# Kernel optimization log

Hardware: AMD Instinct MI355X
Metric: run time of the kernel (lower is better)

Reference implementation:

```python
import jax, jax.numpy as jnp
import numpy as np

N, T, H, F, NZ, G = 768, 8, 128, 128, 64, 64
D = H + F + NZ  # DecoderFC input dim = 320


def _init(key, shape, scale=0.05):
    return jax.random.normal(key, shape, dtype=jnp.float32) * scale


def setup_inputs() -> dict:
    key = jax.random.key(0)
    ks = jax.random.split(key, 16)
    return dict(
        obsv_4d=jax.random.normal(ks[0], (N, T, 4), jnp.float32),
        noise=jax.random.normal(ks[1], (N, NZ), jnp.float32),
        W_emb=_init(ks[2], (H, 4)), b_emb=jnp.zeros((H,), jnp.float32),
        W_ih=_init(ks[3], (4 * H, H)), W_hh=_init(ks[4], (4 * H, H)),
        b_ih=jnp.zeros((4 * H,), jnp.float32), b_hh=jnp.zeros((4 * H,), jnp.float32),
        Wf1=_init(ks[5], (32, 3)), bf1=jnp.zeros((32,), jnp.float32),
        Wf2=_init(ks[6], (64, 32)), bf2=jnp.zeros((64,), jnp.float32),
        Wf3=_init(ks[7], (F, 64)), bf3=jnp.zeros((F,), jnp.float32),
        Wa=_init(ks[8], (F, H)), ba=jnp.zeros((F,), jnp.float32),
        Wd1=_init(ks[9], (D, D)), bd1=jnp.zeros((D,), jnp.float32),
        Wd2=_init(ks[10], (D // 2, D)), bd2=jnp.zeros((D // 2,), jnp.float32),
        Wd3=_init(ks[11], (D // 4, D // 2)), bd3=jnp.zeros((D // 4,), jnp.float32),
        Wd4=_init(ks[12], (2, D // 4)), bd4=jnp.zeros((2,), jnp.float32),
        n_next=12, group_size=G,
    )


def _lstm_cell(h, c, x, W_ih, W_hh, b_ih, b_hh):
    # PyTorch gate order: i, f, g, o
    z = x @ W_ih.T + h @ W_hh.T + b_ih + b_hh
    i, f, g, o = jnp.split(z, 4, axis=-1)
    c = jax.nn.sigmoid(f) * c + jax.nn.sigmoid(i) * jnp.tanh(g)
    h = jax.nn.sigmoid(o) * jnp.tanh(c)
    return h, c


def _social_features(x_last):
    # x_last: [N,4] = (px, py, vx, vy) at last observed step
    Dx = x_last[:, None, :] - x_last[None, :, :]          # [N,N,4]
    Dp, Dv = Dx[..., :2], Dx[..., 2:]
    l2 = jnp.linalg.norm(Dp, axis=2)                      # pairwise distance
    v = jnp.broadcast_to(x_last[:, None, 2:], Dp.shape)   # velocity of agent i
    cos = jnp.sum(Dp * v, -1) / (jnp.linalg.norm(Dp, axis=2) * jnp.linalg.norm(v, axis=2) + 1e-6)
    ttca = -jnp.sum(Dp * Dv, -1) / (jnp.sum(Dv * Dv, -1) + 1e-6)
    dca = jnp.linalg.norm(Dp + ttca[..., None] * Dv, axis=2)
    return jnp.stack([l2, cos, dca], axis=2)              # [N,N,3]


def _attention(f, h, Wa, ba, group_size):
    # Block-diagonal social attention pooling over equal-size sub-batches.
    n = h.shape[0]
    B = n // group_size
    Wh = h @ Wa.T + ba                                    # [N,F]
    fg = f.reshape(B, group_size, B, group_size, -1)
    fg = fg[jnp.arange(B), :, jnp.arange(B)]              # [B,G,G,F] diag blocks
    Whg = Wh.reshape(B, group_size, -1)
    hg = h.reshape(B, group_size, -1)
    sigma = jnp.einsum('bijf,bjf->bij', fg, Whg)          # [B,G,G]
    eye = jnp.eye(group_size, dtype=bool)
    sigma = jnp.where(eye[None], -1000.0, sigma)          # mask self, as in torch code
    attn = jax.nn.softmax(sigma, axis=2)
    S = jnp.einsum('bij,bjh->bih', attn, hg)              # [B,G,H]
    return S.reshape(n, -1)


def reference(obsv_4d, noise, W_emb, b_emb, W_ih, W_hh, b_ih, b_hh,
              Wf1, bf1, Wf2, bf2, Wf3, bf3, Wa, ba,
              Wd1, bd1, Wd2, bd2, Wd3, bd3, Wd4, bd4, n_next, group_size):
    n = obsv_4d.shape[0]
    hdim = W_hh.shape[1]
    # ---- encoder LSTM over observed trajectory ----
    x = obsv_4d @ W_emb.T + b_emb                         # [N,T,H]

    def enc_step(carry, xt):
        h, c = carry
        h, c = _lstm_cell(h, c, xt, W_ih, W_hh, b_ih, b_hh)
        return (h, c), None

    h0 = jnp.zeros((n, hdim), x.dtype)
    (h, c), _ = jax.lax.scan(enc_step, (h0, h0), jnp.swapaxes(x, 0, 1))
    # ---- social features + embedding + attention pooling ----
    feats = _social_features(obsv_4d[:, -1])              # [N,N,3]
    e = jax.nn.relu(feats @ Wf1.T + bf1)
    e = jax.nn.relu(e @ Wf2.T + bf2)
    f = e @ Wf3.T + bf3                                   # [N,N,F]
    weighted = _attention(f, h, Wa, ba, group_size)       # [N,H]
    lrelu = lambda u: jnp.where(u >= 0, u, 0.2 * u)

    def dec_fc(inp):
        u = lrelu(inp @ Wd1.T + bd1)
        u = lrelu(u @ Wd2.T + bd2)
        u = u @ Wd3.T + bd3
        return u @ Wd4.T + bd4

    def dec_step(carry, _):
        h, c, last = carry
        v = dec_fc(jnp.concatenate([h, weighted, noise], axis=1))  # [N,2]
        p = v + last[:, :2]
        new_last = jnp.concatenate([p, v], axis=1)                 # [N,4]
        xe = new_last @ W_emb.T + b_emb
        h, c = _lstm_cell(h, c, xe, W_ih, W_hh, b_ih, b_hh)
        return (h, c, new_last), new_last

    _, preds = jax.lax.scan(dec_step, (h, c, obsv_4d[:, -1]), None, length=n_next)
    return jnp.swapaxes(preds, 0, 1)                      # [N, n_next, 4]
```

## Files before the change

### kernel.cpp

```cpp
#include <hip/hip_runtime.h>
#include <math.h>

#define H_OFF    0
#define C_OFF    98304
#define G_OFF    196608
#define S0_OFF   245760
#define WTD_OFF  246528
#define TIH_OFF  344832
#define THH_OFF  410368
#define TWA_OFF  475904
#define BZ_OFF   492288
#define PKD1_OFF 492800
#define PKD2_OFF 544000
#define PKD3_OFF 569600
#define PKIH_OFF 576000
#define PKHH_OFF 608768

typedef short s8v __attribute__((ext_vector_type(8)));
typedef float f4v __attribute__((ext_vector_type(4)));

__device__ __forceinline__ float sigm(float x) { return 1.0f / (1.0f + __expf(-x)); }
__device__ __forceinline__ float ftanh(float x) { return 1.0f - 2.0f / (__expf(2.0f * x) + 1.0f); }
__device__ __forceinline__ float lrelu(float u) { return u >= 0.f ? u : 0.2f * u; }

__device__ __forceinline__ unsigned bf16rn(float f) {
  unsigned u = __float_as_uint(f);
  return (u + 0x7fffu + ((u >> 16) & 1u)) >> 16;
}
__device__ __forceinline__ unsigned pack2(float a, float b) {
  return bf16rn(a) | (bf16rn(b) << 16);
}
__device__ __forceinline__ int fidx(int a, int k) {
  int kt = k >> 5, kk = k & 31, half = kk >> 4, rem = kk & 15;
  return (kt * 64 + (rem >> 2) * 16 + a) * 8 + half * 4 + (rem & 3);
}

__device__ __forceinline__ void packB(const float* __restrict__ W, int K, int KT,
                                      unsigned* __restrict__ dst, int idx) {
  int t = idx >> 8, r = idx & 255, lane = r >> 2, d = r & 3;
  int nt = t / KT, kt = t % KT;
  int n = nt * 16 + (lane & 15), g = lane >> 4;
  int e0 = 2 * d, e1 = 2 * d + 1;
  int k0 = kt * 32 + ((e0 >> 2) << 4) + g * 4 + (e0 & 3);
  int k1 = kt * 32 + ((e1 >> 2) << 4) + g * 4 + (e1 & 3);
  dst[idx] = pack2(W[(size_t)n * K + k0], W[(size_t)n * K + k1]);
}

__global__ __launch_bounds__(256) void k_tr(
    const float* __restrict__ Wih, const float* __restrict__ Whh,
    const float* __restrict__ Wd1, const float* __restrict__ Wd2,
    const float* __restrict__ Wd3, const float* __restrict__ Wa,
    const float* __restrict__ bih, const float* __restrict__ bhh,
    float* __restrict__ ws)
{
  const int idx = blockIdx.x * 256 + threadIdx.x;
  unsigned* wsu = (unsigned*)ws;
  if (idx < 65536) {
    int j = idx & 3, r = (idx >> 2) & 511, kc = idx >> 11;
    ws[TIH_OFF + idx] = Wih[(size_t)r * 128 + kc * 4 + j];
    ws[THH_OFF + idx] = Whh[(size_t)r * 128 + kc * 4 + j];
  }
  if (idx < 16384) { int k = idx >> 7, r = idx & 127; ws[TWA_OFF + idx] = Wa[(size_t)r * 128 + k]; }
  if (idx < 512)   ws[BZ_OFF + idx] = bih[idx] + bhh[idx];
  if (idx < 51200) packB(Wd1, 320, 10, wsu + PKD1_OFF, idx);
  if (idx < 25600) packB(Wd2, 320, 10, wsu + PKD2_OFF, idx);
  if (idx < 6400)  packB(Wd3, 160, 5,  wsu + PKD3_OFF, idx);
  if (idx < 32768) {
    packB(Wih, 128, 4, wsu + PKIH_OFF, idx);
    packB(Whh, 128, 4, wsu + PKHH_OFF, idx);
  }
}

__global__ __launch_bounds__(512) void k_enc(
    const float* __restrict__ obsv, const float* __restrict__ Wemb,
    const float* __restrict__ bemb, float* __restrict__ ws)
{
  __shared__ float hS[3][128], cS[3][128], zS[3][512], xeS[3][128];
  __shared__ float WembS[512], bembS[128];
  const int tid = threadIdx.x;
  const int wid = tid >> 6, lane = tid & 63;
  const int n0 = blockIdx.x * 3;
  const int row = wid * 64 + lane;

  WembS[tid] = Wemb[tid];
  if (tid < 128) bembS[tid] = bemb[tid];
  if (tid < 384) { int a = tid >> 7, j = tid & 127; hS[a][j] = 0.f; cS[a][j] = 0.f; }
  __syncthreads();

  const float bzv = ws[BZ_OFF + row];
  const float4* wih4 = (const float4*)(ws + TIH_OFF) + row;
  const float4* whh4 = (const float4*)(ws + THH_OFF) + row;

#define FMA4(acc_, w_, x_) acc_ += w_.x*x_.x + w_.y*x_.y + w_.z*x_.z + w_.w*x_.w
  for (int step = 0; step < 8; ++step) {
    if (tid < 384) {
      int a = tid >> 7, j = tid & 127;
      float4 ob = *(const float4*)&obsv[((size_t)(n0 + a) * 8 + step) * 4];
      float4 w = *(const float4*)&WembS[j * 4];
      xeS[a][j] = bembS[j] + ob.x * w.x + ob.y * w.y + ob.z * w.z + ob.w * w.w;
    }
    __syncthreads();
    float a0 = bzv, a1 = bzv, a2 = bzv;
#pragma unroll 4
    for (int kc = 0; kc < 32; ++kc) {
      float4 w = wih4[kc * 512];
      float4 x0 = *(const float4*)&xeS[0][kc * 4];
      float4 x1 = *(const float4*)&xeS[1][kc * 4];
      float4 x2 = *(const float4*)&xeS[2][kc * 4];
      FMA4(a0, w, x0); FMA4(a1, w, x1); FMA4(a2, w, x2);
    }
    if (step > 0) {
#pragma unroll 4
      for (int kc = 0; kc < 32; ++kc) {
        float4 w = whh4[kc * 512];
        float4 h0 = *(const float4*)&hS[0][kc * 4];
        float4 h1 = *(const float4*)&hS[1][kc * 4];
        float4 h2 = *(const float4*)&hS[2][kc * 4];
        FMA4(a0, w, h0); FMA4(a1, w, h1); FMA4(a2, w, h2);
      }
    }
    zS[0][row] = a0; zS[1][row] = a1; zS[2][row] = a2;
    __syncthreads();
    if (tid < 384) {
      int a = tid >> 7, j = tid & 127;
      float ci = sigm(zS[a][j + 128]) * cS[a][j] + sigm(zS[a][j]) * tanhf(zS[a][j + 256]);
      cS[a][j] = ci;
      hS[a][j] = sigm(zS[a][j + 384]) * tanhf(ci);
    }
    __syncthreads();
  }
  if (tid < 384) {
    int a = tid >> 7, j = tid & 127;
    ws[H_OFF + (size_t)(n0 + a) * 128 + j] = hS[a][j];
    ws[C_OFF + (size_t)(n0 + a) * 128 + j] = cS[a][j];
  }
}

__global__ __launch_bounds__(128) void k_social(
    const float* __restrict__ ba, const float* __restrict__ Wf3,
    const float* __restrict__ bf3, float* __restrict__ ws)
{
  __shared__ float hsh[128];
  __shared__ float Wh[128];
  const int n = blockIdx.x, t = threadIdx.x;
  hsh[t] = ws[H_OFF + (size_t)n * 128 + t];
  __syncthreads();
  float acc = ba[t];
#pragma unroll 8
  for (int k = 0; k < 128; ++k) acc += ws[TWA_OFF + (size_t)k * 128 + t] * hsh[k];
  Wh[t] = acc;
  __syncthreads();
  if (t < 64) {
    float g = 0.f;
#pragma unroll 8
    for (int f = 0; f < 128; ++f) g += Wf3[(size_t)f * 64 + t] * Wh[f];
    ws[G_OFF + (size_t)n * 64 + t] = g;
  } else {
    int l = t - 64;
    float p = bf3[l] * Wh[l] + bf3[l + 64] * Wh[l + 64];
    for (int off = 32; off > 0; off >>= 1) p += __shfl_xor(p, off);
    if (l == 0) ws[S0_OFF + n] = p;
  }
}

__global__ __launch_bounds__(64) void k_attn(
    const float* __restrict__ obsv, const float* __restrict__ Wf1,
    const float* __restrict__ bf1, const float* __restrict__ Wf2,
    const float* __restrict__ bf2, float* __restrict__ ws)
{
  __shared__ float w1[96];
  __shared__ float b1[32];
  __shared__ float w2[2048];
  __shared__ float b2[64];
  __shared__ float attn_s[64];
  __shared__ float xi[4];

  const int i = blockIdx.x;
  const int b = i >> 6;
  const int lane = threadIdx.x;
  const int jn = (b << 6) + lane;

  for (int e = lane; e < 96; e += 64) w1[e] = Wf1[e];
  if (lane < 32) b1[lane] = bf1[lane];
  for (int e = lane; e < 2048; e += 64) w2[e] = Wf2[e];
  b2[lane] = bf2[lane];
  if (lane < 4) xi[lane] = obsv[((size_t)i * 8 + 7) * 4 + lane];
  __syncthreads();

  float4 xj = *(const float4*)&obsv[((size_t)jn * 8 + 7) * 4];
  float dpx = xi[0] - xj.x, dpy = xi[1] - xj.y;
  float vix = xi[2], viy = xi[3];
  float dvx = vix - xj.z, dvy = viy - xj.w;
  float l2 = sqrtf(dpx * dpx + dpy * dpy);
  float vnorm = sqrtf(vix * vix + viy * viy);
  float cosv = (dpx * vix + dpy * viy) / (l2 * vnorm + 1e-6f);
  float dv2 = dvx * dvx + dvy * dvy;
  float ttca = -(dpx * dvx + dpy * dvy) / (dv2 + 1e-6f);
  float cax = dpx + ttca * dvx, cay = dpy + ttca * dvy;
  float dca = sqrtf(cax * cax + cay * cay);

  float e1[32];
#pragma unroll
  for (int r = 0; r < 32; ++r)
    e1[r] = fmaxf(w1[r * 3 + 0] * l2 + w1[r * 3 + 1] * cosv + w1[r * 3 + 2] * dca + b1[r], 0.f);

  const float* gp = &ws[G_OFF + (size_t)jn * 64];
  float sig = ws[S0_OFF + jn];
  for (int r = 0; r < 64; ++r) {
    float a2 = b2[r];
#pragma unroll
    for (int k4 = 0; k4 < 8; ++k4) {
      float4 w = *(const float4*)&w2[r * 32 + k4 * 4];
      a2 += w.x * e1[k4 * 4 + 0] + w.y * e1[k4 * 4 + 1] + w.z * e1[k4 * 4 + 2] + w.w * e1[k4 * 4 + 3];
    }
    a2 = fmaxf(a2, 0.f);
    sig += a2 * gp[r];
  }
  if (lane == (i & 63)) sig = -1000.f;

  float m = sig;
  for (int off = 32; off > 0; off >>= 1) m = fmaxf(m, __shfl_xor(m, off));
  float ex = __expf(sig - m);
  float ssum = ex;
  for (int off = 32; off > 0; off >>= 1) ssum += __shfl_xor(ssum, off);
  attn_s[lane] = ex / ssum;
  __syncthreads();

  const float* hbase = &ws[H_OFF + (size_t)(b << 6) * 128];
  float s0a = 0.f, s1a = 0.f;
  for (int j = 0; j < 64; ++j) {
    float aj = attn_s[j];
    s0a += aj * hbase[(size_t)j * 128 + lane];
    s1a += aj * hbase[(size_t)j * 128 + 64 + lane];
  }
  ws[WTD_OFF + (size_t)i * 128 + lane] = s0a;
  ws[WTD_OFF + (size_t)i * 128 + 64 + lane] = s1a;
}

__global__ __launch_bounds__(512) void k_dec(
    const float* __restrict__ obsv, const float* __restrict__ noise,
    const float* __restrict__ Wemb, const float* __restrict__ bemb,
    const float* __restrict__ bd1, const float* __restrict__ bd2,
    const float* __restrict__ bd3, const float* __restrict__ bd4,
    const float* __restrict__ Wd4, const float* __restrict__ bih,
    const float* __restrict__ bhh,
    float* __restrict__ ws, float* __restrict__ out)
{
  __shared__ __align__(16) unsigned short hF0[4 * 64 * 8];
  __shared__ __align__(16) unsigned short hF1[4 * 64 * 8];
  __shared__ __align__(16) unsigned short swF[6 * 64 * 8];
  __shared__ __align__(16) unsigned short u1F[10 * 64 * 8];
  __shared__ __align__(16) unsigned short u2F[5 * 64 * 8];
  __shared__ __align__(16) unsigned short xeF[4 * 64 * 8];
  __shared__ float u3S[16 * 84];
  __shared__ float lastS[64];
  __shared__ float Wd4S[160], bd4S2[2];
  __shared__ float WembS[512], bembS[128];
  __shared__ float bd1S[320], bd2S[160], bd3S[80];

  const int tid = threadIdx.x;
  const int wid = tid >> 6, lane = tid & 63;
  const int n0 = blockIdx.x * 16;
  const int la = lane & 15, lg = lane >> 4;
  const int abase = lg * 4;

  const unsigned* pkd1 = (const unsigned*)(ws) + PKD1_OFF;
  const unsigned* pkd2 = (const unsigned*)(ws) + PKD2_OFF;
  const unsigned* pkd3 = (const unsigned*)(ws) + PKD3_OFF;
  const unsigned* pkih = (const unsigned*)(ws) + PKIH_OFF;
  const unsigned* pkhh = (const unsigned*)(ws) + PKHH_OFF;

  {
    int a = tid & 15, jj = tid >> 4;
#pragma unroll 4
    for (int p = 0; p < 4; ++p) {
      int j = jj + 32 * p;
      hF0[fidx(a, j)] = (unsigned short)bf16rn(ws[H_OFF + (size_t)(n0 + a) * 128 + j]);
      swF[fidx(a, j)] = (unsigned short)bf16rn(ws[WTD_OFF + (size_t)(n0 + a) * 128 + j]);
    }
#pragma unroll 2
    for (int p = 0; p < 2; ++p) {
      int j = jj + 32 * p;
      swF[fidx(a, 128 + j)] = (unsigned short)bf16rn(noise[(size_t)(n0 + a) * 64 + j]);
    }
  }
  if (tid < 64) lastS[tid] = obsv[((size_t)(n0 + (tid >> 2)) * 8 + 7) * 4 + (tid & 3)];
  if (tid < 160) Wd4S[tid] = Wd4[tid];
  if (tid < 2) bd4S2[tid] = bd4[tid];
  WembS[tid] = Wemb[tid];
  if (tid < 128) bembS[tid] = bemb[tid];
  if (tid < 320) bd1S[tid] = bd1[tid];
  if (tid < 160) bd2S[tid] = bd2[tid];
  if (tid < 80) bd3S[tid] = bd3[tid];

  f4v cReg;
  {
    int j = wid * 16 + la;
#pragma unroll
    for (int r = 0; r < 4; ++r)
      cReg[r] = ws[C_OFF + (size_t)(n0 + abase + r) * 128 + j];
  }
  float bzR[4];
#pragma unroll
  for (int t = 0; t < 4; ++t) { int n = (wid + 8 * t) * 16 + la; bzR[t] = bih[n] + bhh[n]; }
  __syncthreads();

  for (int s = 0; s < 12; ++s) {
    unsigned short* hCur = (s & 1) ? hF1 : hF0;
    unsigned short* hNxt = (s & 1) ? hF0 : hF1;

    {
      s8v Av[10];
#pragma unroll
      for (int kt = 0; kt < 4; ++kt) Av[kt] = *(const s8v*)&hCur[(kt * 64 + lane) * 8];
#pragma unroll
      for (int kt = 0; kt < 6; ++kt) Av[4 + kt] = *(const s8v*)&swF[(kt * 64 + lane) * 8];
      for (int nt = wid; nt < 20; nt += 8) {
        s8v Bv[10];
#pragma unroll
        for (int kt = 0; kt < 10; ++kt)
          Bv[kt] = *(const s8v*)(pkd1 + ((size_t)(nt * 10 + kt) * 64 + lane) * 4);
        f4v acc = {0.f, 0.f, 0.f, 0.f};
#pragma unroll
        for (int kt = 0; kt < 10; ++kt)
          acc = __builtin_amdgcn_mfma_f32_16x16x32_bf16(Av[kt], Bv[kt], acc, 0, 0, 0);
        int n = nt * 16 + la;
        float bias = bd1S[n];
#pragma unroll
        for (int r = 0; r < 4; ++r)
          u1F[fidx(abase + r, n)] = (unsigned short)bf16rn(lrelu(acc[r] + bias));
      }
    }
    __syncthreads();
    {
      s8v Av[10];
#pragma unroll
      for (int kt = 0; kt < 10; ++kt) Av[kt] = *(const s8v*)&u1F[(kt * 64 + lane) * 8];
      for (int nt = wid; nt < 10; nt += 8) {
        s8v Bv[10];
#pragma unroll
        for (int kt = 0; kt < 10; ++kt)
          Bv[kt] = *(const s8v*)(pkd2 + ((size_t)(nt * 10 + kt) * 64 + lane) * 4);
        f4v acc = {0.f, 0.f, 0.f, 0.f};
#pragma unroll
        for (int kt = 0; kt < 10; ++kt)
          acc = __builtin_amdgcn_mfma_f32_16x16x32_bf16(Av[kt], Bv[kt], acc, 0, 0, 0);
        int n = nt * 16 + la;
        float bias = bd2S[n];
#pragma unroll
        for (int r = 0; r < 4; ++r)
          u2F[fidx(abase + r, n)] = (unsigned short)bf16rn(lrelu(acc[r] + bias));
      }
    }
    __syncthreads();
    if (wid < 5) {
      s8v Av[5], Bv[5];
#pragma unroll
      for (int kt = 0; kt < 5; ++kt) {
        Av[kt] = *(const s8v*)&u2F[(kt * 64 + lane) * 8];
        Bv[kt] = *(const s8v*)(pkd3 + ((size_t)(wid * 5 + kt) * 64 + lane) * 4);
      }
      f4v acc = {0.f, 0.f, 0.f, 0.f};
#pragma unroll
      for (int kt = 0; kt < 5; ++kt)
        acc = __builtin_amdgcn_mfma_f32_16x16x32_bf16(Av[kt], Bv[kt], acc, 0, 0, 0);
      int n = wid * 16 + la;
      float bias = bd3S[n];
#pragma unroll
      for (int r = 0; r < 4; ++r)
        u3S[(abase + r) * 84 + n] = acc[r] + bias;
    }
    __syncthreads();
    if (tid < 128) {
      int a = tid >> 3, r = (tid >> 2) & 1, q = tid & 3;
      float part = 0.f;
#pragma unroll
      for (int i = q * 20; i < q * 20 + 20; ++i)
        part += Wd4S[r * 80 + i] * u3S[a * 84 + i];
      part += __shfl_xor(part, 1);
      part += __shfl_xor(part, 2);
      if (q == 0) {
        float v = part + bd4S2[r];
        float p = v + lastS[a * 4 + r];
        lastS[a * 4 + r] = p;
        lastS[a * 4 + 2 + r] = v;
        out[(size_t)(n0 + a) * 48 + s * 4 + r] = p;
        out[(size_t)(n0 + a) * 48 + s * 4 + 2 + r] = v;
      }
    }
    __syncthreads();
    {
      int a = tid & 15, jj = tid >> 4;
      float l0 = lastS[a * 4 + 0], l1 = lastS[a * 4 + 1];
      float l2v = lastS[a * 4 + 2], l3 = lastS[a * 4 + 3];
#pragma unroll
      for (int p = 0; p < 4; ++p) {
        int j = jj + 32 * p;
        float4 w = *(const float4*)&WembS[j * 4];
        float xv = bembS[j] + l0 * w.x + l1 * w.y + l2v * w.z + l3 * w.w;
        xeF[fidx(a, j)] = (unsigned short)bf16rn(xv);
      }
    }
    __syncthreads();
#define ZQUAD(Q, ZN)                                                              \
    f4v ZN = {0.f, 0.f, 0.f, 0.f};                                                \
    {                                                                             \
      const int nt = wid + 8 * (Q);                                               \
      s8v Bv[4];                                                                  \
      _Pragma("unroll")                                                           \
      for (int kt = 0; kt < 4; ++kt)                                              \
        Bv[kt] = *(const s8v*)(pkih + ((size_t)(nt * 4 + kt) * 64 + lane) * 4);   \
      _Pragma("unroll")                                                           \
      for (int kt = 0; kt < 4; ++kt)                                              \
        ZN = __builtin_amdgcn_mfma_f32_16x16x32_bf16(                             \
            *(const s8v*)&xeF[(kt * 64 + lane) * 8], Bv[kt], ZN, 0, 0, 0);        \
      _Pragma("unroll")                                                           \
      for (int kt = 0; kt < 4; ++kt)                                              \
        Bv[kt] = *(const s8v*)(pkhh + ((size_t)(nt * 4 + kt) * 64 + lane) * 4);   \
      _Pragma("unroll")                                                           \
      for (int kt = 0; kt < 4; ++kt)                                              \
        ZN = __builtin_amdgcn_mfma_f32_16x16x32_bf16(                             \
            *(const s8v*)&hCur[(kt * 64 + lane) * 8], Bv[kt], ZN, 0, 0, 0);       \
    }                                                                             \
    __builtin_amdgcn_sched_barrier(0);

    {
      ZQUAD(0, z0)
      ZQUAD(1, z1)
      ZQUAD(2, z2)
      ZQUAD(3, z3)
      int j = wid * 16 + la;
#pragma unroll
      for (int r = 0; r < 4; ++r) {
        float ci = sigm(z1[r] + bzR[1]) * cReg[r]
                 + sigm(z0[r] + bzR[0]) * ftanh(z2[r] + bzR[2]);
        cReg[r] = ci;
        float hv = sigm(z3[r] + bzR[3]) * ftanh(ci);
        hNxt[fidx(abase + r, j)] = (unsigned short)bf16rn(hv);
      }
    }
#undef ZQUAD
    __syncthreads();
  }
}

extern "C" void kernel_launch(void* const* d_in, const int* in_sizes, int n_in,
                              void* d_out, int out_size, void* d_ws, size_t ws_size,
                              hipStream_t stream)
{
  const float* obsv = (const float*)d_in[0];
  const float* noise = (const float*)d_in[1];
  const float* Wemb = (const float*)d_in[2];
  const float* bemb = (const float*)d_in[3];
  const float* Wih = (const float*)d_in[4];
  const float* Whh = (const float*)d_in[5];
  const float* bih = (const float*)d_in[6];
  const float* bhh = (const float*)d_in[7];
  const float* Wf1 = (const float*)d_in[8];
  const float* bf1 = (const float*)d_in[9];
  const float* Wf2 = (const float*)d_in[10];
  const float* bf2 = (const float*)d_in[11];
  const float* Wf3 = (const float*)d_in[12];
  const float* bf3 = (const float*)d_in[13];
  const float* Wa = (const float*)d_in[14];
  const float* ba = (const float*)d_in[15];
  const float* Wd1 = (const float*)d_in[16];
  const float* bd1 = (const float*)d_in[17];
  const float* Wd2 = (const float*)d_in[18];
  const float* bd2 = (const float*)d_in[19];
  const float* Wd3 = (const float*)d_in[20];
  const float* bd3 = (const float*)d_in[21];
  const float* Wd4 = (const float*)d_in[22];
  const float* bd4 = (const float*)d_in[23];
  float* ws = (float*)d_ws;
  float* out = (float*)d_out;

  k_tr<<<256, 256, 0, stream>>>(Wih, Whh, Wd1, Wd2, Wd3, Wa, bih, bhh, ws);
  k_enc<<<256, 512, 0, stream>>>(obsv, Wemb, bemb, ws);
  k_social<<<768, 128, 0, stream>>>(ba, Wf3, bf3, ws);
  k_attn<<<768, 64, 0, stream>>>(obsv, Wf1, bf1, Wf2, bf2, ws);
  k_dec<<<48, 512, 0, stream>>>(obsv, noise, Wemb, bemb, bd1, bd2, bd3, bd4, Wd4,
                                bih, bhh, ws, out);
}
```

Measured before the change: 186.3 us.

## Rewrite encoder LSTM with bf16 MFMA over 16-agent tiles

The encoder LSTM moves from fp32 scalar FMAs with 3 agents per block (256 blocks) to bf16 MFMA 16x16x32 tiles with 16 agents per block (48 blocks). It reuses the packed Wih/Whh fragments that the decoder already uses. The fp32 transposed weight and bias copies in the transpose kernel are dropped, and that kernel's grid shrinks. The decoder's first MLP layers also read A fragments straight from LDS instead of preloading them into registers, which lowers register pressure. This trades encoder precision for bf16, and fewer blocks means lower GPU occupancy.

After: 163.6 us. -12.2%, faster.

```diff
diff --git a/kernel.cpp b/kernel.cpp
--- a/kernel.cpp
+++ b/kernel.cpp
@@ -6,10 +6,7 @@
 #define G_OFF    196608
 #define S0_OFF   245760
 #define WTD_OFF  246528
-#define TIH_OFF  344832
-#define THH_OFF  410368
 #define TWA_OFF  475904
-#define BZ_OFF   492288
 #define PKD1_OFF 492800
 #define PKD2_OFF 544000
 #define PKD3_OFF 569600
@@ -50,18 +47,11 @@
     const float* __restrict__ Wih, const float* __restrict__ Whh,
     const float* __restrict__ Wd1, const float* __restrict__ Wd2,
     const float* __restrict__ Wd3, const float* __restrict__ Wa,
-    const float* __restrict__ bih, const float* __restrict__ bhh,
     float* __restrict__ ws)
 {
   const int idx = blockIdx.x * 256 + threadIdx.x;
   unsigned* wsu = (unsigned*)ws;
-  if (idx < 65536) {
-    int j = idx & 3, r = (idx >> 2) & 511, kc = idx >> 11;
-    ws[TIH_OFF + idx] = Wih[(size_t)r * 128 + kc * 4 + j];
-    ws[THH_OFF + idx] = Whh[(size_t)r * 128 + kc * 4 + j];
-  }
   if (idx < 16384) { int k = idx >> 7, r = idx & 127; ws[TWA_OFF + idx] = Wa[(size_t)r * 128 + k]; }
-  if (idx < 512)   ws[BZ_OFF + idx] = bih[idx] + bhh[idx];
   if (idx < 51200) packB(Wd1, 320, 10, wsu + PKD1_OFF, idx);
   if (idx < 25600) packB(Wd2, 320, 10, wsu + PKD2_OFF, idx);
   if (idx < 6400)  packB(Wd3, 160, 5,  wsu + PKD3_OFF, idx);
@@ -71,68 +61,99 @@
   }
 }
 
+#define ZQUAD(Q, ZN, XEBUF, HBUF)                                                 \
+    f4v ZN = {0.f, 0.f, 0.f, 0.f};                                               \
+    {                                                                             \
+      const int nt = wid + 8 * (Q);                                               \
+      s8v Bv[4];                                                                  \
+      _Pragma("unroll")                                                           \
+      for (int kt = 0; kt < 4; ++kt)                                              \
+        Bv[kt] = *(const s8v*)(pkih + ((size_t)(nt * 4 + kt) * 64 + lane) * 4);   \
+      _Pragma("unroll")                                                           \
+      for (int kt = 0; kt < 4; ++kt)                                              \
+        ZN = __builtin_amdgcn_mfma_f32_16x16x32_bf16(                             \
+            *(const s8v*)&XEBUF[(kt * 64 + lane) * 8], Bv[kt], ZN, 0, 0, 0);      \
+      _Pragma("unroll")                                                           \
+      for (int kt = 0; kt < 4; ++kt)                                              \
+        Bv[kt] = *(const s8v*)(pkhh + ((size_t)(nt * 4 + kt) * 64 + lane) * 4);   \
+      _Pragma("unroll")                                                           \
+      for (int kt = 0; kt < 4; ++kt)                                              \
+        ZN = __builtin_amdgcn_mfma_f32_16x16x32_bf16(                             \
+            *(const s8v*)&HBUF[(kt * 64 + lane) * 8], Bv[kt], ZN, 0, 0, 0);       \
+    }                                                                             \
+    __builtin_amdgcn_sched_barrier(0);
+
 __global__ __launch_bounds__(512) void k_enc(
     const float* __restrict__ obsv, const float* __restrict__ Wemb,
-    const float* __restrict__ bemb, float* __restrict__ ws)
-{
-  __shared__ float hS[3][128], cS[3][128], zS[3][512], xeS[3][128];
+    const float* __restrict__ bemb, const float* __restrict__ bih,
+    const float* __restrict__ bhh, float* __restrict__ ws)
+{
+  __shared__ __align__(16) unsigned short hF0[4 * 64 * 8];
+  __shared__ __align__(16) unsigned short hF1[4 * 64 * 8];
+  __shared__ __align__(16) unsigned short xeF[4 * 64 * 8];
   __shared__ float WembS[512], bembS[128];
+  __shared__ float obS[16][32];
+
   const int tid = threadIdx.x;
   const int wid = tid >> 6, lane = tid & 63;
-  const int n0 = blockIdx.x * 3;
-  const int row = wid * 64 + lane;
+  const int n0 = blockIdx.x * 16;
+  const int la = lane & 15, lg = lane >> 4;
+  const int abase = lg * 4;
+
+  const unsigned* pkih = (const unsigned*)(ws) + PKIH_OFF;
+  const unsigned* pkhh = (const unsigned*)(ws) + PKHH_OFF;
 
   WembS[tid] = Wemb[tid];
   if (tid < 128) bembS[tid] = bemb[tid];
-  if (tid < 384) { int a = tid >> 7, j = tid & 127; hS[a][j] = 0.f; cS[a][j] = 0.f; }
-  __syncthreads();
-
-  const float bzv = ws[BZ_OFF + row];
-  const float4* wih4 = (const float4*)(ws + TIH_OFF) + row;
-  const float4* whh4 = (const float4*)(ws + THH_OFF) + row;
-
-#define FMA4(acc_, w_, x_) acc_ += w_.x*x_.x + w_.y*x_.y + w_.z*x_.z + w_.w*x_.w
+  {
+    int a = tid >> 5, td = tid & 31;
+    obS[a][td] = obsv[(size_t)(n0 + a) * 32 + td];
+  }
+  for (int e = tid; e < 2048; e += 512) hF0[e] = 0;
+
+  f4v cReg = {0.f, 0.f, 0.f, 0.f};
+  float bzR[4];
+#pragma unroll
+  for (int t = 0; t < 4; ++t) { int n = (wid + 8 * t) * 16 + la; bzR[t] = bih[n] + bhh[n]; }
+  __syncthreads();
+
   for (int step = 0; step < 8; ++step) {
-    if (tid < 384) {
-      int a = tid >> 7, j = tid & 127;
-      float4 ob = *(const float4*)&obsv[((size_t)(n0 + a) * 8 + step) * 4];
-      float4 w = *(const float4*)&WembS[j * 4];
-      xeS[a][j] = bembS[j] + ob.x * w.x + ob.y * w.y + ob.z * w.z + ob.w * w.w;
-    }
-    __syncthreads();
-    float a0 = bzv, a1 = bzv, a2 = bzv;
-#pragma unroll 4
-    for (int kc = 0; kc < 32; ++kc) {
-      float4 w = wih4[kc * 512];
-      float4 x0 = *(const float4*)&xeS[0][kc * 4];
-      float4 x1 = *(const float4*)&xeS[1][kc * 4];
-      float4 x2 = *(const float4*)&xeS[2][kc * 4];
-      FMA4(a0, w, x0); FMA4(a1, w, x1); FMA4(a2, w, x2);
-    }
-    if (step > 0) {
-#pragma unroll 4
-      for (int kc = 0; kc < 32; ++kc) {
-        float4 w = whh4[kc * 512];
-        float4 h0 = *(const float4*)&hS[0][kc * 4];
-        float4 h1 = *(const float4*)&hS[1][kc * 4];
-        float4 h2 = *(const float4*)&hS[2][kc * 4];
-        FMA4(a0, w, h0); FMA4(a1, w, h1); FMA4(a2, w, h2);
+    unsigned short* hCur = (step & 1) ? hF1 : hF0;
+    unsigned short* hNxt = (step & 1) ? hF0 : hF1;
+
+    {
+      int a = tid & 15, jj = tid >> 4;
+      float l0 = obS[a][step * 4 + 0], l1 = obS[a][step * 4 + 1];
+      float l2v = obS[a][step * 4 + 2], l3 = obS[a][step * 4 + 3];
+#pragma unroll
+      for (int p = 0; p < 4; ++p) {
+        int j = jj + 32 * p;
+        float4 w = *(const float4*)&WembS[j * 4];
+        float xv = bembS[j] + l0 * w.x + l1 * w.y + l2v * w.z + l3 * w.w;
+        xeF[fidx(a, j)] = (unsigned short)bf16rn(xv);
       }
     }
-    zS[0][row] = a0; zS[1][row] = a1; zS[2][row] = a2;
-    __syncthreads();
-    if (tid < 384) {
-      int a = tid >> 7, j = tid & 127;
-      float ci = sigm(zS[a][j + 128]) * cS[a][j] + sigm(zS[a][j]) * tanhf(zS[a][j + 256]);
-      cS[a][j] = ci;
-      hS[a][j] = sigm(zS[a][j + 384]) * tanhf(ci);
-    }
-    __syncthreads();
-  }
-  if (tid < 384) {
-    int a = tid >> 7, j = tid & 127;
-    ws[H_OFF + (size_t)(n0 + a) * 128 + j] = hS[a][j];
-    ws[C_OFF + (size_t)(n0 + a) * 128 + j] = cS[a][j];
+    __syncthreads();
+    {
+      ZQUAD(0, z0, xeF, hCur)
+      ZQUAD(1, z1, xeF, hCur)
+      ZQUAD(2, z2, xeF, hCur)
+      ZQUAD(3, z3, xeF, hCur)
+      int j = wid * 16 + la;
+#pragma unroll
+      for (int r = 0; r < 4; ++r) {
+        float ci = sigm(z1[r] + bzR[1]) * cReg[r]
+                 + sigm(z0[r] + bzR[0]) * ftanh(z2[r] + bzR[2]);
+        cReg[r] = ci;
+        float hv = sigm(z3[r] + bzR[3]) * ftanh(ci);
+        hNxt[fidx(abase + r, j)] = (unsigned short)bf16rn(hv);
+        if (step == 7) {
+          ws[H_OFF + (size_t)(n0 + abase + r) * 128 + j] = hv;
+          ws[C_OFF + (size_t)(n0 + abase + r) * 128 + j] = ci;
+        }
+      }
+    }
+    __syncthreads();
   }
 }
 
@@ -309,61 +330,52 @@
     unsigned short* hCur = (s & 1) ? hF1 : hF0;
     unsigned short* hNxt = (s & 1) ? hF0 : hF1;
 
-    {
-      s8v Av[10];
-#pragma unroll
-      for (int kt = 0; kt < 4; ++kt) Av[kt] = *(const s8v*)&hCur[(kt * 64 + lane) * 8];
-#pragma unroll
-      for (int kt = 0; kt < 6; ++kt) Av[4 + kt] = *(const s8v*)&swF[(kt * 64 + lane) * 8];
-      for (int nt = wid; nt < 20; nt += 8) {
-        s8v Bv[10];
-#pragma unroll
-        for (int kt = 0; kt < 10; ++kt)
-          Bv[kt] = *(const s8v*)(pkd1 + ((size_t)(nt * 10 + kt) * 64 + lane) * 4);
-        f4v acc = {0.f, 0.f, 0.f, 0.f};
-#pragma unroll
-        for (int kt = 0; kt < 10; ++kt)
-          acc = __builtin_amdgcn_mfma_f32_16x16x32_bf16(Av[kt], Bv[kt], acc, 0, 0, 0);
-        int n = nt * 16 + la;
-        float bias = bd1S[n];
-#pragma unroll
-        for (int r = 0; r < 4; ++r)
-          u1F[fidx(abase + r, n)] = (unsigned short)bf16rn(lrelu(acc[r] + bias));
-      }
-    }
-    __syncthreads();
-    {
-      s8v Av[10];
-#pragma unroll
-      for (int kt = 0; kt < 10; ++kt) Av[kt] = *(const s8v*)&u1F[(kt * 64 + lane) * 8];
-      for (int nt = wid; nt < 10; nt += 8) {
-        s8v Bv[10];
-#pragma unroll
-        for (int kt = 0; kt < 10; ++kt)
-          Bv[kt] = *(const s8v*)(pkd2 + ((size_t)(nt * 10 + kt) * 64 + lane) * 4);
-        f4v acc = {0.f, 0.f, 0.f, 0.f};
-#pragma unroll
-        for (int kt = 0; kt < 10; ++kt)
-          acc = __builtin_amdgcn_mfma_f32_16x16x32_bf16(Av[kt], Bv[kt], acc, 0, 0, 0);
-        int n = nt * 16 + la;
-        float bias = bd2S[n];
-#pragma unroll
-        for (int r = 0; r < 4; ++r)
-          u2F[fidx(abase + r, n)] = (unsigned short)bf16rn(lrelu(acc[r] + bias));
-      }
+#define A320(kt) (*(const s8v*)((kt) < 4 ? &hCur[((kt) * 64 + lane) * 8] : &swF[(((kt) - 4) * 64 + lane) * 8]))
+
+    for (int nt = wid; nt < 20; nt += 8) {
+      s8v Bv[10];
+#pragma unroll
+      for (int kt = 0; kt < 10; ++kt)
+        Bv[kt] = *(const s8v*)(pkd1 + ((size_t)(nt * 10 + kt) * 64 + lane) * 4);
+      f4v acc = {0.f, 0.f, 0.f, 0.f};
+#pragma unroll
+      for (int kt = 0; kt < 10; ++kt)
+        acc = __builtin_amdgcn_mfma_f32_16x16x32_bf16(A320(kt), Bv[kt], acc, 0, 0, 0);
+      int n = nt * 16 + la;
+      float bias = bd1S[n];
+#pragma unroll
+      for (int r = 0; r < 4; ++r)
+        u1F[fidx(abase + r, n)] = (unsigned short)bf16rn(lrelu(acc[r] + bias));
+    }
+#undef A320
+    __syncthreads();
+    for (int nt = wid; nt < 10; nt += 8) {
+      s8v Bv[10];
+#pragma unroll
+      for (int kt = 0; kt < 10; ++kt)
+        Bv[kt] = *(const s8v*)(pkd2 + ((size_t)(nt * 10 + kt) * 64 + lane) * 4);
+      f4v acc = {0.f, 0.f, 0.f, 0.f};
+#pragma unroll
+      for (int kt = 0; kt < 10; ++kt)
+        acc = __builtin_amdgcn_mfma_f32_16x16x32_bf16(
+            *(const s8v*)&u1F[(kt * 64 + lane) * 8], Bv[kt], acc, 0, 0, 0);
+      int n = nt * 16 + la;
+      float bias = bd2S[n];
+#pragma unroll
+      for (int r = 0; r < 4; ++r)
+        u2F[fidx(abase + r, n)] = (unsigned short)bf16rn(lrelu(acc[r] + bias));
     }
     __syncthreads();
     if (wid < 5) {
-      s8v Av[5], Bv[5];
-#pragma unroll
-      for (int kt = 0; kt < 5; ++kt) {
-        Av[kt] = *(const s8v*)&u2F[(kt * 64 + lane) * 8];
+      s8v Bv[5];
+#pragma unroll
+      for (int kt = 0; kt < 5; ++kt)
         Bv[kt] = *(const s8v*)(pkd3 + ((size_t)(wid * 5 + kt) * 64 + lane) * 4);
-      }
       f4v acc = {0.f, 0.f, 0.f, 0.f};
 #pragma unroll
       for (int kt = 0; kt < 5; ++kt)
-        acc = __builtin_amdgcn_mfma_f32_16x16x32_bf16(Av[kt], Bv[kt], acc, 0, 0, 0);
+        acc = __builtin_amdgcn_mfma_f32_16x16x32_bf16(
+            *(const s8v*)&u2F[(kt * 64 + lane) * 8], Bv[kt], acc, 0, 0, 0);
       int n = wid * 16 + la;
       float bias = bd3S[n];
 #pragma unroll
@@ -402,33 +414,11 @@
       }
     }
     __syncthreads();
-#define ZQUAD(Q, ZN)                                                              \
-    f4v ZN = {0.f, 0.f, 0.f, 0.f};                                                \
-    {                                                                             \
-      const int nt = wid + 8 * (Q);                                               \
-      s8v Bv[4];                                                                  \
-      _Pragma("unroll")                                                           \
-      for (int kt = 0; kt < 4; ++kt)                                              \
-        Bv[kt] = *(const s8v*)(pkih + ((size_t)(nt * 4 + kt) * 64 + lane) * 4);   \
-      _Pragma("unroll")                                                           \
-      for (int kt = 0; kt < 4; ++kt)                                              \
-        ZN = __builtin_amdgcn_mfma_f32_16x16x32_bf16(                             \
-            *(const s8v*)&xeF[(kt * 64 + lane) * 8], Bv[kt], ZN, 0, 0, 0);        \
-      _Pragma("unroll")                                                           \
-      for (int kt = 0; kt < 4; ++kt)                                              \
-        Bv[kt] = *(const s8v*)(pkhh + ((size_t)(nt * 4 + kt) * 64 + lane) * 4);   \
-      _Pragma("unroll")                                                           \
-      for (int kt = 0; kt < 4; ++kt)                                              \
-        ZN = __builtin_amdgcn_mfma_f32_16x16x32_bf16(                             \
-            *(const s8v*)&hCur[(kt * 64 + lane) * 8], Bv[kt], ZN, 0, 0, 0);       \
-    }                                                                             \
-    __builtin_amdgcn_sched_barrier(0);
-
     {
-      ZQUAD(0, z0)
-      ZQUAD(1, z1)
-      ZQUAD(2, z2)
-      ZQUAD(3, z3)
+      ZQUAD(0, z0, xeF, hCur)
+      ZQUAD(1, z1, xeF, hCur)
+      ZQUAD(2, z2, xeF, hCur)
+      ZQUAD(3, z3, xeF, hCur)
       int j = wid * 16 + la;
 #pragma unroll
       for (int r = 0; r < 4; ++r) {
@@ -439,7 +429,6 @@
         hNxt[fidx(abase + r, j)] = (unsigned short)bf16rn(hv);
       }
     }
-#undef ZQUAD
     __syncthreads();
   }
 }
@@ -475,8 +464,8 @@
   float* ws = (float*)d_ws;
   float* out = (float*)d_out;
 
-  k_tr<<<256, 256, 0, stream>>>(Wih, Whh, Wd1, Wd2, Wd3, Wa, bih, bhh, ws);
-  k_enc<<<256, 512, 0, stream>>>(obsv, Wemb, bemb, ws);
+  k_tr<<<200, 256, 0, stream>>>(Wih, Whh, Wd1, Wd2, Wd3, Wa, ws);
+  k_enc<<<48, 512, 0, stream>>>(obsv, Wemb, bemb, bih, bhh, ws);
   k_social<<<768, 128, 0, stream>>>(ba, Wf3, bf3, ws);
   k_attn<<<768, 64, 0, stream>>>(obsv, Wf1, bf1, Wf2, bf2, ws);
   k_dec<<<48, 512, 0, stream>>>(obsv, noise, Wemb, bemb, bd1, bd2, bd3, bd4, Wd4,
```
